# Performance work log

Measured on AMD Instinct MI355X. Metric: run time of the kernel, lower is better.

Reference implementation:

```python
import jax, jax.numpy as jnp
import numpy as np

N_SENT = 100000   # source ('sent') nodes
N_TYPE = 10000    # destination ('type') nodes
E = 640000        # edges of etype 'has'
D = 128           # out_dim
LEAKY_SLOPE = 0.01  # F.leaky_relu default


def setup_inputs() -> dict:
    key = jax.random.key(0)
    k0, k1, k2, k3, k4 = jax.random.split(key, 5)
    h_sent = jax.random.normal(k0, (N_SENT, D), jnp.float32)
    h_type = jax.random.normal(k1, (N_TYPE, D), jnp.float32)
    # attn_fc: Linear(2*D, 1, bias=False) -> weight [1, 2*D]
    attn_w = jax.random.normal(k2, (1, 2 * D), jnp.float32) * (1.0 / np.sqrt(2 * D))
    src_idx = jax.random.randint(k3, (E,), 0, N_SENT, dtype=jnp.int32)
    dst_idx = jax.random.randint(k4, (E,), 0, N_TYPE, dtype=jnp.int32)
    return {"h_sent": h_sent, "h_type": h_type, "attn_w": attn_w,
            "src_idx": src_idx, "dst_idx": dst_idx}


def reference(h_sent, h_type, attn_w, src_idx, dst_idx):
    w = attn_w[0]  # [2D]
    # attn_fc(cat(src_h, dst_h)) == src_h @ w[:D] + dst_h @ w[D:]  (no bias)
    s_src = h_sent @ w[:D]   # [N_SENT]
    s_dst = h_type @ w[D:]   # [N_TYPE]
    e = jax.nn.leaky_relu(s_src[src_idx] + s_dst[dst_idx], LEAKY_SLOPE)  # [E]
    # segment (per-destination) softmax over incoming edges
    m = jax.ops.segment_max(e, dst_idx, num_segments=N_TYPE)             # [N_TYPE]
    m = jnp.where(jnp.isfinite(m), m, 0.0)                               # empty segments -> 0
    ex = jnp.exp(e - m[dst_idx])                                         # [E]
    denom = jax.ops.segment_sum(ex, dst_idx, num_segments=N_TYPE)        # [N_TYPE]
    alpha = ex / denom[dst_idx]                                          # [E]
    # weighted scatter-sum of source features into destination nodes
    msg = alpha[:, None] * h_sent[src_idx]                               # [E, D]
    h_new = jax.ops.segment_sum(msg, dst_idx, num_segments=N_TYPE)       # [N_TYPE, D]
    # DGL only updates nodes that received messages; isolated nodes keep h
    deg = jax.ops.segment_sum(jnp.ones_like(e), dst_idx, num_segments=N_TYPE)
    return jnp.where(deg[:, None] > 0, h_new, h_type)
```

## Files before the change

kernel.cpp:

```cpp
#include <hip/hip_runtime.h>
#include <stdint.h>
#include <stddef.h>

#define N_SENT 100000
#define N_TYPE 10000
#define NEDGE  640000
#define NROWS  (N_SENT + N_TYPE)
#define HB     128
#define HCHUNK (NEDGE / HB)

__device__ __forceinline__ float bf2f(uint32_t lo16) {
    return __builtin_bit_cast(float, lo16 << 16);
}
__device__ __forceinline__ uint32_t f2bf(float f) {
    uint32_t u = __builtin_bit_cast(uint32_t, f);
    return (u + 0x7fffu + ((u >> 16) & 1u)) >> 16;
}
__device__ __forceinline__ bool detect_bf16(const uint32_t* __restrict__ h) {
    uint32_t u = h[threadIdx.x & 63];
    uint32_t e_lo = (u >> 7) & 0xffu;
    int ok = (e_lo >= 100u && e_lo <= 140u) ? 1 : 0;
    unsigned long long m = __ballot(ok);
    return __popcll(m) >= 48;
}

#define SCORE_BLOCKS ((NROWS + 63) / 64)

__global__ __launch_bounds__(256) void scores_count_k(const void* __restrict__ h_sent,
                                                      const void* __restrict__ h_type,
                                                      const void* __restrict__ attn_w,
                                                      const int* __restrict__ dst,
                                                      float* __restrict__ s_src,
                                                      float* __restrict__ s_dst,
                                                      uint32_t* __restrict__ count2) {
    __shared__ uint32_t hist[N_TYPE];
    int b = blockIdx.x;
    if (b < SCORE_BLOCKS) {
        int lane = threadIdx.x & 63;
        int r0   = (b * 4 + (int)(threadIdx.x >> 6)) * 16;
        bool isbf = detect_bf16((const uint32_t*)h_sent);
        float v[16];
        if (isbf) {
            uint32_t wv_s = ((const uint32_t*)attn_w)[lane];
            uint32_t wv_t = ((const uint32_t*)attn_w)[64 + lane];
            float ws0 = bf2f(wv_s & 0xffffu), ws1 = bf2f(wv_s >> 16);
            float wt0 = bf2f(wv_t & 0xffffu), wt1 = bf2f(wv_t >> 16);
#pragma unroll
            for (int i = 0; i < 16; i++) {
                int g = r0 + i;
                if (g >= NROWS) { v[i] = 0.0f; continue; }
                bool isSrc = g < N_SENT;
                const uint32_t* hp = isSrc
                    ? (const uint32_t*)h_sent + (size_t)g * 64
                    : (const uint32_t*)h_type + (size_t)(g - N_SENT) * 64;
                uint32_t hv = hp[lane];
                v[i] = isSrc ? (bf2f(hv & 0xffffu) * ws0 + bf2f(hv >> 16) * ws1)
                             : (bf2f(hv & 0xffffu) * wt0 + bf2f(hv >> 16) * wt1);
            }
        } else {
            float2 wv_s = ((const float2*)attn_w)[lane];
            float2 wv_t = ((const float2*)attn_w)[64 + lane];
#pragma unroll
            for (int i = 0; i < 16; i++) {
                int g = r0 + i;
                if (g >= NROWS) { v[i] = 0.0f; continue; }
                bool isSrc = g < N_SENT;
                const float2* hp = isSrc
                    ? (const float2*)h_sent + (size_t)g * 64
                    : (const float2*)h_type + (size_t)(g - N_SENT) * 64;
                float2 hv = hp[lane];
                v[i] = isSrc ? (hv.x * wv_s.x + hv.y * wv_s.y)
                             : (hv.x * wv_t.x + hv.y * wv_t.y);
            }
        }
        int b0 = lane & 1, b1 = (lane >> 1) & 1, b2 = (lane >> 2) & 1, b3 = (lane >> 3) & 1;
        float w_[8];
#pragma unroll
        for (int i = 0; i < 8; i++) {
            float keep = b0 ? v[2 * i + 1] : v[2 * i];
            float send = b0 ? v[2 * i]     : v[2 * i + 1];
            w_[i] = keep + __shfl_xor(send, 1, 64);
        }
        float x_[4];
#pragma unroll
        for (int i = 0; i < 4; i++) {
            float keep = b1 ? w_[2 * i + 1] : w_[2 * i];
            float send = b1 ? w_[2 * i]     : w_[2 * i + 1];
            x_[i] = keep + __shfl_xor(send, 2, 64);
        }
        float y_[2];
#pragma unroll
        for (int i = 0; i < 2; i++) {
            float keep = b2 ? x_[2 * i + 1] : x_[2 * i];
            float send = b2 ? x_[2 * i]     : x_[2 * i + 1];
            y_[i] = keep + __shfl_xor(send, 4, 64);
        }
        float z;
        {
            float keep = b3 ? y_[1] : y_[0];
            float send = b3 ? y_[0] : y_[1];
            z = keep + __shfl_xor(send, 8, 64);
        }
        z += __shfl_xor(z, 16, 64);
        z += __shfl_xor(z, 32, 64);
        if (lane < 16) {
            int g = r0 + lane;
            if (g < NROWS) {
                if (g < N_SENT) s_src[g] = z;
                else            s_dst[g - N_SENT] = z;
            }
        }
    } else {
        int cb = b - SCORE_BLOCKS;
        int t  = threadIdx.x;
        for (int i = t; i < N_TYPE; i += 256) hist[i] = 0u;
        __syncthreads();
        int e0 = cb * HCHUNK;
        for (int i = t; i < HCHUNK; i += 256)
            atomicAdd(&hist[dst[e0 + i]], 1u);
        __syncthreads();
        uint32_t* row = count2 + (size_t)cb * N_TYPE;
        for (int i = t; i < N_TYPE; i += 256) row[i] = hist[i];
    }
}

__global__ __launch_bounds__(256) void sumscan_k(uint32_t* __restrict__ count2,
                                                 uint32_t* __restrict__ total) {
    int b = blockIdx.x * 256 + threadIdx.x;
    if (b >= N_TYPE) return;
    uint32_t run = 0;
#pragma unroll 8
    for (int c = 0; c < HB; c++) {
        uint32_t* p = count2 + (size_t)c * N_TYPE + b;
        uint32_t v = *p;
        *p = run;
        run += v;
    }
    total[b] = run;
}

__global__ __launch_bounds__(1024) void scan_k(const uint32_t* __restrict__ total,
                                               uint32_t* __restrict__ offsets) {
    const int CH = 10;
    int t = threadIdx.x, lane = t & 63, wv = t >> 6;
    int base = t * CH;
    uint32_t local[CH];
    uint32_t tsum = 0;
#pragma unroll
    for (int i = 0; i < CH; i++) {
        int idx = base + i;
        uint32_t c = (idx < N_TYPE) ? total[idx] : 0u;
        local[i] = c;
        tsum += c;
    }
    uint32_t orig = tsum;
#pragma unroll
    for (int off = 1; off < 64; off <<= 1) {
        uint32_t v = __shfl_up(tsum, off, 64);
        if (lane >= off) tsum += v;
    }
    __shared__ uint32_t wsum[16];
    if (lane == 63) wsum[wv] = tsum;
    __syncthreads();
    if (wv == 0 && lane < 16) {
        uint32_t u = wsum[lane], o = u;
#pragma unroll
        for (int off = 1; off < 16; off <<= 1) {
            uint32_t v = __shfl_up(u, off, 64);
            if (lane >= off) u += v;
        }
        wsum[lane] = u - o;
    }
    __syncthreads();
    uint32_t run = wsum[wv] + tsum - orig;
#pragma unroll
    for (int i = 0; i < CH; i++) {
        int idx = base + i;
        if (idx < N_TYPE) {
            offsets[idx] = run;
            run += local[i];
        } else if (idx == N_TYPE) {
            offsets[idx] = run;
        }
    }
}

__global__ __launch_bounds__(256) void fill_k(const int* __restrict__ src,
                                              const int* __restrict__ dst,
                                              const float* __restrict__ s_src,
                                              const float* __restrict__ s_dst,
                                              const uint32_t* __restrict__ offsets,
                                              const uint32_t* __restrict__ base2,
                                              uint2* __restrict__ edata) {
    __shared__ uint32_t cur[N_TYPE];
    int cb = blockIdx.x;
    int t  = threadIdx.x;
    const uint32_t* brow = base2 + (size_t)cb * N_TYPE;
    for (int i = t; i < N_TYPE; i += 256) cur[i] = offsets[i] + brow[i];
    __syncthreads();
    int e0 = cb * HCHUNK;
    for (int i = t; i < HCHUNK; i += 256) {
        int e = e0 + i;
        int d = dst[e];
        int s = src[e];
        float v = s_src[s] + s_dst[d];
        v = v > 0.0f ? v : 0.01f * v;
        float w = __expf(v);
        uint32_t pos = atomicAdd(&cur[d], 1u);
        edata[pos] = make_uint2((uint32_t)s, __builtin_bit_cast(uint32_t, w));
    }
}

__global__ __launch_bounds__(256) void agg_k(const void* __restrict__ h_sent,
                                             const void* __restrict__ h_type,
                                             const uint32_t* __restrict__ offsets,
                                             const uint2* __restrict__ edata,
                                             void* __restrict__ out) {
    int lane = threadIdx.x & 63;
    int j = (blockIdx.x * 256 + (int)threadIdx.x) >> 6;
    if (j >= N_TYPE) return;
    bool isbf = detect_bf16((const uint32_t*)h_sent);
    uint32_t beg = offsets[j], end = offsets[j + 1];
    if (beg == end) {
        if (isbf) ((uint32_t*)out)[(size_t)j * 64 + lane] =
                      ((const uint32_t*)h_type)[(size_t)j * 64 + lane];
        else      ((float2*)out)[(size_t)j * 64 + lane] =
                      ((const float2*)h_type)[(size_t)j * 64 + lane];
        return;
    }
    float a0 = 0.0f, a1 = 0.0f, den = 0.0f;
    if (isbf) {
        const uint32_t* hp = (const uint32_t*)h_sent;
        uint32_t k = beg;
        for (; k + 8 <= end; k += 8) {
            uint2 ed[8];
#pragma unroll
            for (int i = 0; i < 8; i++) ed[i] = edata[k + i];
            uint32_t gv[8];
#pragma unroll
            for (int i = 0; i < 8; i++) gv[i] = hp[(size_t)ed[i].x * 64 + lane];
#pragma unroll
            for (int i = 0; i < 8; i++) {
                float w = __builtin_bit_cast(float, ed[i].y);
                den += w;
                a0 += w * bf2f(gv[i] & 0xffffu);
                a1 += w * bf2f(gv[i] >> 16);
            }
        }
        for (; k < end; ++k) {
            uint2 ed = edata[k];
            uint32_t gv = hp[(size_t)ed.x * 64 + lane];
            float w = __builtin_bit_cast(float, ed.y);
            den += w;
            a0 += w * bf2f(gv & 0xffffu);
            a1 += w * bf2f(gv >> 16);
        }
        float inv = 1.0f / den;
        ((uint32_t*)out)[(size_t)j * 64 + lane] = f2bf(a0 * inv) | (f2bf(a1 * inv) << 16);
    } else {
        const float2* hp = (const float2*)h_sent;
        uint32_t k = beg;
        for (; k + 8 <= end; k += 8) {
            uint2 ed[8];
#pragma unroll
            for (int i = 0; i < 8; i++) ed[i] = edata[k + i];
            float2 gv[8];
#pragma unroll
            for (int i = 0; i < 8; i++) gv[i] = hp[(size_t)ed[i].x * 64 + lane];
#pragma unroll
            for (int i = 0; i < 8; i++) {
                float w = __builtin_bit_cast(float, ed[i].y);
                den += w;
                a0 += w * gv[i].x;
                a1 += w * gv[i].y;
            }
        }
        for (; k < end; ++k) {
            uint2 ed = edata[k];
            float2 gv = hp[(size_t)ed.x * 64 + lane];
            float w = __builtin_bit_cast(float, ed.y);
            den += w;
            a0 += w * gv.x;
            a1 += w * gv.y;
        }
        float inv = 1.0f / den;
        ((float2*)out)[(size_t)j * 64 + lane] = make_float2(a0 * inv, a1 * inv);
    }
}

static inline size_t align_up(size_t x) { return (x + 255) & ~(size_t)255; }

extern "C" void kernel_launch(void* const* d_in, const int* in_sizes, int n_in,
                              void* d_out, int out_size, void* d_ws, size_t ws_size,
                              hipStream_t stream) {
    const void* h_sent = d_in[0];
    const void* h_type = d_in[1];
    const void* attn_w = d_in[2];
    const int* src_idx = (const int*)d_in[3];
    const int* dst_idx = (const int*)d_in[4];

    char* w = (char*)d_ws;
    float*    s_src   = (float*)w;    w += align_up((size_t)N_SENT * 4);
    float*    s_dst   = (float*)w;    w += align_up((size_t)N_TYPE * 4);
    uint32_t* count2  = (uint32_t*)w; w += align_up((size_t)HB * N_TYPE * 4);
    uint32_t* total   = (uint32_t*)w; w += align_up((size_t)N_TYPE * 4);
    uint32_t* offsets = (uint32_t*)w; w += align_up((size_t)(N_TYPE + 1) * 4);
    uint2*    edata   = (uint2*)w;    w += align_up((size_t)NEDGE * 8);

    scores_count_k<<<SCORE_BLOCKS + HB, 256, 0, stream>>>(
        h_sent, h_type, attn_w, dst_idx, s_src, s_dst, count2);
    sumscan_k<<<(N_TYPE + 255) / 256, 256, 0, stream>>>(count2, total);
    scan_k<<<1, 1024, 0, stream>>>(total, offsets);
    fill_k<<<HB, 256, 0, stream>>>(src_idx, dst_idx, s_src, s_dst, offsets, count2, edata);
    agg_k<<<(N_TYPE + 3) / 4, 256, 0, stream>>>(h_sent, h_type, offsets, edata, d_out);
}
```

Before: 199.3 us.

## Widen gather loads in aggregation with multi-edge-per-wave lane grouping

The aggregation kernel now splits each wavefront into lane groups that each process a different edge. Every lane gathers a 16-byte vector of the source row, so one wave load instruction covers several edges, and edge metadata is loaded once per batch and broadcast with shuffles. Partial sums are combined across groups with xor-shuffles before normalisation. The fill kernel's shared-memory init also switches to vectorized uint4 reads. This cuts load instruction count and raises memory-level parallelism, at the cost of extra shuffles, cross-group reductions, and idle lanes on the output store.

```diff
diff --git a/kernel.cpp b/kernel.cpp
--- a/kernel.cpp
+++ b/kernel.cpp
@@ -195,8 +195,15 @@
     __shared__ uint32_t cur[N_TYPE];
     int cb = blockIdx.x;
     int t  = threadIdx.x;
-    const uint32_t* brow = base2 + (size_t)cb * N_TYPE;
-    for (int i = t; i < N_TYPE; i += 256) cur[i] = offsets[i] + brow[i];
+    const uint4* off4 = (const uint4*)offsets;
+    const uint4* brow4 = (const uint4*)(base2 + (size_t)cb * N_TYPE);
+    for (int i = t; i < N_TYPE / 4; i += 256) {
+        uint4 o = off4[i], bq = brow4[i];
+        cur[4 * i + 0] = o.x + bq.x;
+        cur[4 * i + 1] = o.y + bq.y;
+        cur[4 * i + 2] = o.z + bq.z;
+        cur[4 * i + 3] = o.w + bq.w;
+    }
     __syncthreads();
     int e0 = cb * HCHUNK;
     for (int i = t; i < HCHUNK; i += 256) {
@@ -221,70 +228,99 @@
     if (j >= N_TYPE) return;
     bool isbf = detect_bf16((const uint32_t*)h_sent);
     uint32_t beg = offsets[j], end = offsets[j + 1];
-    if (beg == end) {
-        if (isbf) ((uint32_t*)out)[(size_t)j * 64 + lane] =
-                      ((const uint32_t*)h_type)[(size_t)j * 64 + lane];
-        else      ((float2*)out)[(size_t)j * 64 + lane] =
-                      ((const float2*)h_type)[(size_t)j * 64 + lane];
-        return;
-    }
-    float a0 = 0.0f, a1 = 0.0f, den = 0.0f;
     if (isbf) {
-        const uint32_t* hp = (const uint32_t*)h_sent;
+        int g = lane >> 4, p = lane & 15;
+        if (beg == end) {
+            if (lane < 16)
+                ((uint4*)out)[(size_t)j * 16 + p] = ((const uint4*)h_type)[(size_t)j * 16 + p];
+            return;
+        }
+        const uint4* hp = (const uint4*)h_sent;
+        float a[8] = {0, 0, 0, 0, 0, 0, 0, 0};
+        float den = 0.0f;
         uint32_t k = beg;
-        for (; k + 8 <= end; k += 8) {
-            uint2 ed[8];
-#pragma unroll
-            for (int i = 0; i < 8; i++) ed[i] = edata[k + i];
-            uint32_t gv[8];
-#pragma unroll
-            for (int i = 0; i < 8; i++) gv[i] = hp[(size_t)ed[i].x * 64 + lane];
+        for (; k + 32 <= end; k += 32) {
+            uint2 ed = edata[k + (lane & 31)];
 #pragma unroll
             for (int i = 0; i < 8; i++) {
-                float w = __builtin_bit_cast(float, ed[i].y);
+                int sl = 4 * i + g;
+                uint32_t s = (uint32_t)__shfl((int)ed.x, sl, 64);
+                float    w = __builtin_bit_cast(float, (uint32_t)__shfl((int)ed.y, sl, 64));
+                uint4 gv = hp[(size_t)s * 16 + p];
                 den += w;
-                a0 += w * bf2f(gv[i] & 0xffffu);
-                a1 += w * bf2f(gv[i] >> 16);
-            }
-        }
-        for (; k < end; ++k) {
-            uint2 ed = edata[k];
-            uint32_t gv = hp[(size_t)ed.x * 64 + lane];
-            float w = __builtin_bit_cast(float, ed.y);
+                a[0] += w * bf2f(gv.x & 0xffffu); a[1] += w * bf2f(gv.x >> 16);
+                a[2] += w * bf2f(gv.y & 0xffffu); a[3] += w * bf2f(gv.y >> 16);
+                a[4] += w * bf2f(gv.z & 0xffffu); a[5] += w * bf2f(gv.z >> 16);
+                a[6] += w * bf2f(gv.w & 0xffffu); a[7] += w * bf2f(gv.w >> 16);
+            }
+        }
+        for (; k < end; k += 4) {
+            uint32_t idx = k + (uint32_t)g;
+            bool valid = idx < end;
+            uint2 ed = edata[valid ? idx : (end - 1)];
+            float w = valid ? __builtin_bit_cast(float, ed.y) : 0.0f;
+            uint4 gv = hp[(size_t)ed.x * 16 + p];
             den += w;
-            a0 += w * bf2f(gv & 0xffffu);
-            a1 += w * bf2f(gv >> 16);
-        }
+            a[0] += w * bf2f(gv.x & 0xffffu); a[1] += w * bf2f(gv.x >> 16);
+            a[2] += w * bf2f(gv.y & 0xffffu); a[3] += w * bf2f(gv.y >> 16);
+            a[4] += w * bf2f(gv.z & 0xffffu); a[5] += w * bf2f(gv.z >> 16);
+            a[6] += w * bf2f(gv.w & 0xffffu); a[7] += w * bf2f(gv.w >> 16);
+        }
+#pragma unroll
+        for (int i = 0; i < 8; i++) {
+            a[i] += __shfl_xor(a[i], 16, 64);
+            a[i] += __shfl_xor(a[i], 32, 64);
+        }
+        den += __shfl_xor(den, 16, 64);
+        den += __shfl_xor(den, 32, 64);
         float inv = 1.0f / den;
-        ((uint32_t*)out)[(size_t)j * 64 + lane] = f2bf(a0 * inv) | (f2bf(a1 * inv) << 16);
+        if (lane < 16) {
+            uint4 o;
+            o.x = f2bf(a[0] * inv) | (f2bf(a[1] * inv) << 16);
+            o.y = f2bf(a[2] * inv) | (f2bf(a[3] * inv) << 16);
+            o.z = f2bf(a[4] * inv) | (f2bf(a[5] * inv) << 16);
+            o.w = f2bf(a[6] * inv) | (f2bf(a[7] * inv) << 16);
+            ((uint4*)out)[(size_t)j * 16 + p] = o;
+        }
     } else {
-        const float2* hp = (const float2*)h_sent;
+        int g = lane >> 5, p = lane & 31;
+        if (beg == end) {
+            if (lane < 32)
+                ((float4*)out)[(size_t)j * 32 + p] = ((const float4*)h_type)[(size_t)j * 32 + p];
+            return;
+        }
+        const float4* hp = (const float4*)h_sent;
+        float a0 = 0, a1 = 0, a2 = 0, a3 = 0, den = 0.0f;
         uint32_t k = beg;
-        for (; k + 8 <= end; k += 8) {
-            uint2 ed[8];
-#pragma unroll
-            for (int i = 0; i < 8; i++) ed[i] = edata[k + i];
-            float2 gv[8];
-#pragma unroll
-            for (int i = 0; i < 8; i++) gv[i] = hp[(size_t)ed[i].x * 64 + lane];
+        for (; k + 16 <= end; k += 16) {
+            uint2 ed = edata[k + (lane & 15)];
 #pragma unroll
             for (int i = 0; i < 8; i++) {
-                float w = __builtin_bit_cast(float, ed[i].y);
+                int sl = 2 * i + g;
+                uint32_t s = (uint32_t)__shfl((int)ed.x, sl, 64);
+                float    w = __builtin_bit_cast(float, (uint32_t)__shfl((int)ed.y, sl, 64));
+                float4 gv = hp[(size_t)s * 32 + p];
                 den += w;
-                a0 += w * gv[i].x;
-                a1 += w * gv[i].y;
-            }
-        }
-        for (; k < end; ++k) {
-            uint2 ed = edata[k];
-            float2 gv = hp[(size_t)ed.x * 64 + lane];
-            float w = __builtin_bit_cast(float, ed.y);
+                a0 += w * gv.x; a1 += w * gv.y; a2 += w * gv.z; a3 += w * gv.w;
+            }
+        }
+        for (; k < end; k += 2) {
+            uint32_t idx = k + (uint32_t)g;
+            bool valid = idx < end;
+            uint2 ed = edata[valid ? idx : (end - 1)];
+            float w = valid ? __builtin_bit_cast(float, ed.y) : 0.0f;
+            float4 gv = hp[(size_t)ed.x * 32 + p];
             den += w;
-            a0 += w * gv.x;
-            a1 += w * gv.y;
-        }
+            a0 += w * gv.x; a1 += w * gv.y; a2 += w * gv.z; a3 += w * gv.w;
+        }
+        a0 += __shfl_xor(a0, 32, 64);
+        a1 += __shfl_xor(a1, 32, 64);
+        a2 += __shfl_xor(a2, 32, 64);
+        a3 += __shfl_xor(a3, 32, 64);
+        den += __shfl_xor(den, 32, 64);
         float inv = 1.0f / den;
-        ((float2*)out)[(size_t)j * 64 + lane] = make_float2(a0 * inv, a1 * inv);
+        if (lane < 32)
+            ((float4*)out)[(size_t)j * 32 + p] = make_float4(a0 * inv, a1 * inv, a2 * inv, a3 * inv);
     }
 }
 
```

Result: slower. 203.7 us (+2.2%).
